# Performance work log

Hardware: AMD Instinct MI355X
Metric: run time of the kernel (lower is better)

Reference implementation:

```python
import jax, jax.numpy as jnp
import numpy as np

N_NODES = 100000
N_RELS = 8
N_EDGES = 150000
D_IN = 128
D_OUT = 128


def setup_inputs() -> dict:
    key = jax.random.key(0)
    k1, k2, k3, k4, k5 = jax.random.split(key, 5)
    scale = 1.0 / np.sqrt(D_IN)
    return {
        "x": jax.random.normal(k1, (N_NODES, D_IN), dtype=jnp.float32),
        "weight": jax.random.normal(k2, (N_RELS, D_IN, D_OUT), dtype=jnp.float32) * scale,
        "self_loop_weight": jax.random.normal(k3, (D_IN, D_OUT), dtype=jnp.float32) * scale,
        "bias": jnp.zeros((D_OUT,), dtype=jnp.float32),
        "src": jax.random.randint(k4, (N_RELS, N_EDGES), 0, N_NODES, dtype=jnp.int64),
        "dst": jax.random.randint(k5, (N_RELS, N_EDGES), 0, N_NODES, dtype=jnp.int64),
    }


def reference(x, weight, self_loop_weight, bias, src, dst):
    # Per-relation GraphConv(norm='right'): for each dst node, mean of incoming
    # src features (sum / in-degree, degree clamped to 1), then matmul W_r.
    # HeteroGraphConv sums relation outputs; then self-loop, bias, relu.
    n = x.shape[0]

    def per_rel(s, d, W):
        msgs = jax.ops.segment_sum(x[s], d, num_segments=n)          # [N, D_IN]
        deg = jax.ops.segment_sum(jnp.ones_like(s, dtype=x.dtype), d,
                                  num_segments=n)                     # [N]
        msgs = msgs / jnp.maximum(deg, 1.0)[:, None]
        return msgs @ W                                               # [N, D_OUT]

    agg = jax.vmap(per_rel)(src, dst, weight).sum(axis=0)             # [N, D_OUT]
    out = agg + x @ self_loop_weight + bias
    return jax.nn.relu(out)
```

## Files before the change

kernel.cpp:

```cpp
#include <hip/hip_runtime.h>
#include <hip/hip_bf16.h>
#include <stdint.h>

#define N_NODES 100000
#define N_RELS  8
#define N_EDGES 150000
#define KCOLS   1152
#define CAP     64

typedef short bf16x8 __attribute__((ext_vector_type(8)));
typedef float f32x4  __attribute__((ext_vector_type(4)));

__device__ __forceinline__ unsigned short f2b(float f) {
    union { float f; unsigned u; } v; v.f = f;
    unsigned r = v.u + 0x7FFF + ((v.u >> 16) & 1);
    return (unsigned short)(r >> 16);
}

__global__ void prep_w(const float* __restrict__ W, const float* __restrict__ Wself,
                       unsigned short* __restrict__ BT) {
    int flat = blockIdx.x * 256 + threadIdx.x;
    if (flat >= 128 * KCOLS) return;
    int n = flat / KCOLS, k = flat - n * KCOLS;
    float v;
    if (k < 1024) {
        int r = k >> 7, kk = k & 127;
        v = W[(r << 14) + (kk << 7) + n];
    } else {
        v = Wself[((k - 1024) << 7) + n];
    }
    BT[flat] = f2b(v);
}

__global__ void cast_x(const float* __restrict__ X, unsigned short* __restrict__ xb) {
    int t = blockIdx.x * 256 + threadIdx.x;
    if (t >= N_NODES * 16) return;
    const float4* p = (const float4*)(X + (size_t)t * 8);
    float4 a = p[0], b = p[1];
    unsigned short o[8] = { f2b(a.x), f2b(a.y), f2b(a.z), f2b(a.w),
                            f2b(b.x), f2b(b.y), f2b(b.z), f2b(b.w) };
    *(int4*)(xb + (size_t)t * 8) = *(const int4*)o;
}

__global__ void edge_build(const int* __restrict__ src, const int* __restrict__ dst,
                           int* __restrict__ cnt, int* __restrict__ ebuf) {
    int e = blockIdx.x * 256 + threadIdx.x;
    int r = blockIdx.y;
    if (e >= N_EDGES) return;
    int s = src[r * N_EDGES + e];
    int d = dst[r * N_EDGES + e];
    int slot = atomicAdd(&cnt[d], 1);
    if (slot < CAP) ebuf[d * CAP + slot] = (r << 17) | s;
}

__global__ __launch_bounds__(256) void agg_x(
    const unsigned short* __restrict__ xb, const int* __restrict__ ebuf,
    const int* __restrict__ cnt, unsigned short* __restrict__ Agg) {
    int d = (blockIdx.x << 2) + (threadIdx.x >> 6);
    if (d >= N_NODES) return;
    int lane = threadIdx.x & 63;

    int k = cnt[d]; if (k > CAP) k = CAP;
    int rec = (lane < k) ? ebuf[d * CAP + lane] : -1;
    int rl = rec >> 17;

    const unsigned int* xw = (const unsigned int*)xb;

    unsigned long long mask[8];
#pragma unroll
    for (int r = 0; r < 8; ++r) mask[r] = __ballot(rl == r);

    float ax[8], ay[8];
#pragma unroll
    for (int r = 0; r < 8; ++r) { ax[r] = 0.f; ay[r] = 0.f; }

#pragma unroll
    for (int r = 0; r < 8; ++r) {
        unsigned long long m = mask[r];
        while (m) {
            int idx = (int)__builtin_ctzll(m);
            m &= m - 1;
            int rc = __builtin_amdgcn_readlane(rec, idx);
            int s  = rc & 0x1FFFF;
            unsigned int y2 = xw[(size_t)s * 64 + lane];
            union { unsigned u; float f; } vx, vy;
            vx.u = y2 << 16;
            vy.u = y2 & 0xFFFF0000u;
            ax[r] += vx.f;
            ay[r] += vy.f;
        }
    }

#pragma unroll
    for (int r = 0; r < 8; ++r) {
        int dg = __popcll(mask[r]);
        float invr = 1.0f / (float)(dg < 1 ? 1 : dg);
        unsigned short lo = f2b(ax[r] * invr);
        unsigned short hi = f2b(ay[r] * invr);
        unsigned int pk = (unsigned int)lo | ((unsigned int)hi << 16);
        *(unsigned int*)&Agg[(size_t)d * 1024 + (r << 7) + (lane << 1)] = pk;
    }
}

__global__ __launch_bounds__(256) void gemm_out(
    const unsigned short* __restrict__ Agg, const unsigned short* __restrict__ xb,
    const unsigned short* __restrict__ BT, const float* __restrict__ bias,
    float* __restrict__ out) {
    __shared__ short As[128 * 136];
    __shared__ short Bs[128 * 136];
    int t = threadIdx.x;
    int rowBase = blockIdx.x * 128;

    int w = t >> 6, lane = t & 63;
    int wr = w >> 1, wc = w & 1;
    int ml = lane & 15, quad = lane >> 4;

    f32x4 acc[4][4];
#pragma unroll
    for (int i = 0; i < 4; ++i)
#pragma unroll
        for (int j = 0; j < 4; ++j)
            acc[i][j] = (f32x4){0.f, 0.f, 0.f, 0.f};

    for (int kc = 0; kc < 9; ++kc) {
#pragma unroll
        for (int it = 0; it < 8; ++it) {
            int idx = t + it * 256;
            int row = idx >> 4, c = idx & 15;
            int grow = rowBase + row;
            int4 v = make_int4(0, 0, 0, 0);
            if (grow < N_NODES) {
                if (kc < 8)
                    v = *(const int4*)&Agg[(size_t)grow * 1024 + (kc << 7) + c * 8];
                else
                    v = *(const int4*)&xb[(size_t)grow * 128 + c * 8];
            }
            *(int4*)&As[row * 136 + c * 8] = v;
        }
#pragma unroll
        for (int it = 0; it < 8; ++it) {
            int idx = t + it * 256;
            int n = idx >> 4, c = idx & 15;
            *(int4*)&Bs[n * 136 + c * 8] =
                *(const int4*)&BT[(size_t)n * KCOLS + (kc << 7) + c * 8];
        }
        __syncthreads();

#pragma unroll
        for (int kb = 0; kb < 4; ++kb) {
            int ko = kb * 32 + quad * 8;
            bf16x8 a[4], b[4];
#pragma unroll
            for (int i = 0; i < 4; ++i)
                a[i] = *(const bf16x8*)&As[(wr * 64 + i * 16 + ml) * 136 + ko];
#pragma unroll
            for (int j = 0; j < 4; ++j)
                b[j] = *(const bf16x8*)&Bs[(wc * 64 + j * 16 + ml) * 136 + ko];
#pragma unroll
            for (int i = 0; i < 4; ++i)
#pragma unroll
                for (int j = 0; j < 4; ++j)
                    acc[i][j] = __builtin_amdgcn_mfma_f32_16x16x32_bf16(a[i], b[j], acc[i][j], 0, 0, 0);
        }
        __syncthreads();
    }

#pragma unroll
    for (int i = 0; i < 4; ++i) {
#pragma unroll
        for (int j = 0; j < 4; ++j) {
            int col = wc * 64 + j * 16 + ml;
            float bv = bias[col];
#pragma unroll
            for (int rr = 0; rr < 4; ++rr) {
                int row = rowBase + wr * 64 + i * 16 + quad * 4 + rr;
                if (row < N_NODES) {
                    float v = acc[i][j][rr] + bv;
                    out[(size_t)row * 128 + col] = fmaxf(v, 0.f);
                }
            }
        }
    }
}

extern "C" void kernel_launch(void* const* d_in, const int* in_sizes, int n_in,
                              void* d_out, int out_size, void* d_ws, size_t ws_size,
                              hipStream_t stream) {
    const float* x     = (const float*)d_in[0];
    const float* W     = (const float*)d_in[1];
    const float* Wself = (const float*)d_in[2];
    const float* bias  = (const float*)d_in[3];
    const int*   src   = (const int*)d_in[4];
    const int*   dst   = (const int*)d_in[5];
    float* out = (float*)d_out;

    char* ws = (char*)d_ws;
    size_t off = 0;
    unsigned short* Agg = (unsigned short*)(ws + off); off += (size_t)N_NODES * 1024 * 2;
    unsigned short* xb  = (unsigned short*)(ws + off); off += (size_t)N_NODES * 128 * 2;
    unsigned short* BT  = (unsigned short*)(ws + off); off += (size_t)128 * KCOLS * 2;
    int* cnt  = (int*)(ws + off); off += (size_t)N_NODES * 4;
    int* ebuf = (int*)(ws + off); off += (size_t)N_NODES * CAP * 4;

    hipMemsetAsync(cnt, 0, (size_t)N_NODES * 4, stream);

    prep_w<<<(128 * KCOLS + 255) / 256, 256, 0, stream>>>(W, Wself, BT);
    cast_x<<<(N_NODES * 16 + 255) / 256, 256, 0, stream>>>(x, xb);

    dim3 eg((N_EDGES + 255) / 256, N_RELS);
    edge_build<<<eg, 256, 0, stream>>>(src, dst, cnt, ebuf);

    agg_x<<<(N_NODES + 3) / 4, 256, 0, stream>>>(xb, ebuf, cnt, Agg);

    gemm_out<<<(N_NODES + 127) / 128, 256, 0, stream>>>(Agg, xb, BT, bias, out);
}
```

Before: 390.6 us.

## Double-buffer GEMM tiles via direct global-to-LDS loads with XOR-swizzled layouts

The GEMM now stages its A and B tiles through global_load_lds straight into LDS, with two buffers of 64-wide K halves, so the next tile loads while MFMAs run on the current one. To keep LDS reads free of bank conflicts without padding, the layouts of BT, xb and Agg are XOR-swizzled when they are produced, and the gather in agg_x unswizzles source rows to match. This removes register staging and the serialized load-then-compute step, at the cost of coupling every producer kernel to the swizzle, twice as many K steps and barriers, and clamped out-of-range rows that load real data.

Result: faster. 361.3 us (-7.5%).

```diff
diff --git a/kernel.cpp b/kernel.cpp
--- a/kernel.cpp
+++ b/kernel.cpp
@@ -10,12 +10,21 @@
 
 typedef short bf16x8 __attribute__((ext_vector_type(8)));
 typedef float f32x4  __attribute__((ext_vector_type(4)));
+typedef unsigned int u32;
 
 __device__ __forceinline__ unsigned short f2b(float f) {
     union { float f; unsigned u; } v; v.f = f;
     unsigned r = v.u + 0x7FFF + ((v.u >> 16) & 1);
     return (unsigned short)(r >> 16);
 }
+
+__device__ __forceinline__ void gld16(const void* g, void* lds_uniform) {
+    __builtin_amdgcn_global_load_lds(
+        (const __attribute__((address_space(1))) u32*)g,
+        (__attribute__((address_space(3))) u32*)lds_uniform,
+        16, 0, 0);
+}
+
 
 __global__ void prep_w(const float* __restrict__ W, const float* __restrict__ Wself,
                        unsigned short* __restrict__ BT) {
@@ -29,17 +38,20 @@
     } else {
         v = Wself[((k - 1024) << 7) + n];
     }
-    BT[flat] = f2b(v);
+    int ks = (k & ~63) | ((k & 63) ^ ((n & 7) << 3));
+    BT[(size_t)n * KCOLS + ks] = f2b(v);
 }
 
 __global__ void cast_x(const float* __restrict__ X, unsigned short* __restrict__ xb) {
     int t = blockIdx.x * 256 + threadIdx.x;
     if (t >= N_NODES * 16) return;
-    const float4* p = (const float4*)(X + (size_t)t * 8);
+    int row = t >> 4, g = t & 15;
+    const float4* p = (const float4*)(X + (size_t)row * 128 + g * 8);
     float4 a = p[0], b = p[1];
     unsigned short o[8] = { f2b(a.x), f2b(a.y), f2b(a.z), f2b(a.w),
                             f2b(b.x), f2b(b.y), f2b(b.z), f2b(b.w) };
-    *(int4*)(xb + (size_t)t * 8) = *(const int4*)o;
+    int g2 = (g & 8) | ((g & 7) ^ (row & 7));
+    *(int4*)(xb + (size_t)row * 128 + (g2 << 3)) = *(const int4*)o;
 }
 
 __global__ void edge_build(const int* __restrict__ src, const int* __restrict__ dst,
@@ -82,7 +94,7 @@
             m &= m - 1;
             int rc = __builtin_amdgcn_readlane(rec, idx);
             int s  = rc & 0x1FFFF;
-            unsigned int y2 = xw[(size_t)s * 64 + lane];
+            unsigned int y2 = xw[(size_t)s * 64 + (lane ^ ((s & 7) << 2))];
             union { unsigned u; float f; } vx, vy;
             vx.u = y2 << 16;
             vy.u = y2 & 0xFFFF0000u;
@@ -91,6 +103,7 @@
         }
     }
 
+    int sw = (lane ^ ((d & 7) << 2)) << 1;
 #pragma unroll
     for (int r = 0; r < 8; ++r) {
         int dg = __popcll(mask[r]);
@@ -98,7 +111,7 @@
         unsigned short lo = f2b(ax[r] * invr);
         unsigned short hi = f2b(ay[r] * invr);
         unsigned int pk = (unsigned int)lo | ((unsigned int)hi << 16);
-        *(unsigned int*)&Agg[(size_t)d * 1024 + (r << 7) + (lane << 1)] = pk;
+        *(unsigned int*)&Agg[(size_t)d * 1024 + (r << 7) + sw] = pk;
     }
 }
 
@@ -106,14 +119,18 @@
     const unsigned short* __restrict__ Agg, const unsigned short* __restrict__ xb,
     const unsigned short* __restrict__ BT, const float* __restrict__ bias,
     float* __restrict__ out) {
-    __shared__ short As[128 * 136];
-    __shared__ short Bs[128 * 136];
+    __shared__ short As[2][128 * 64];
+    __shared__ short Bs[2][128 * 64];
     int t = threadIdx.x;
     int rowBase = blockIdx.x * 128;
 
     int w = t >> 6, lane = t & 63;
     int wr = w >> 1, wc = w & 1;
     int ml = lane & 15, quad = lane >> 4;
+    int sa = (lane & 7) << 4;
+
+    int ri = lane >> 3;
+    int cb = (lane & 7) << 4;
 
     f32x4 acc[4][4];
 #pragma unroll
@@ -122,47 +139,54 @@
         for (int j = 0; j < 4; ++j)
             acc[i][j] = (f32x4){0.f, 0.f, 0.f, 0.f};
 
-    for (int kc = 0; kc < 9; ++kc) {
-#pragma unroll
-        for (int it = 0; it < 8; ++it) {
-            int idx = t + it * 256;
-            int row = idx >> 4, c = idx & 15;
+    auto stage = [&](int buf, int t2) {
+        int kc = t2 >> 1, h = t2 & 1;
+#pragma unroll
+        for (int j = 0; j < 4; ++j) {
+            int i = (w << 2) + j;
+            int row = (i << 3) + ri;
             int grow = rowBase + row;
-            int4 v = make_int4(0, 0, 0, 0);
-            if (grow < N_NODES) {
-                if (kc < 8)
-                    v = *(const int4*)&Agg[(size_t)grow * 1024 + (kc << 7) + c * 8];
-                else
-                    v = *(const int4*)&xb[(size_t)grow * 128 + c * 8];
-            }
-            *(int4*)&As[row * 136 + c * 8] = v;
-        }
-#pragma unroll
-        for (int it = 0; it < 8; ++it) {
-            int idx = t + it * 256;
-            int n = idx >> 4, c = idx & 15;
-            *(int4*)&Bs[n * 136 + c * 8] =
-                *(const int4*)&BT[(size_t)n * KCOLS + (kc << 7) + c * 8];
-        }
-        __syncthreads();
-
-#pragma unroll
-        for (int kb = 0; kb < 4; ++kb) {
-            int ko = kb * 32 + quad * 8;
+            if (grow > N_NODES - 1) grow = N_NODES - 1;
+            const char* ga = (kc < 8)
+                ? (const char*)Agg + (size_t)grow * 2048 + (kc << 8) + (h << 7) + cb
+                : (const char*)xb  + (size_t)grow * 256  + (h << 7) + cb;
+            gld16(ga, (char*)&As[buf][0] + (i << 10));
+            const char* gb = (const char*)BT + (size_t)row * 2304 + (t2 << 7) + cb;
+            gld16(gb, (char*)&Bs[buf][0] + (i << 10));
+        }
+    };
+
+    auto compute = [&](int buf) {
+#pragma unroll
+        for (int kb = 0; kb < 2; ++kb) {
+            int off = ((kb << 6) + (quad << 4)) ^ sa;
             bf16x8 a[4], b[4];
 #pragma unroll
             for (int i = 0; i < 4; ++i)
-                a[i] = *(const bf16x8*)&As[(wr * 64 + i * 16 + ml) * 136 + ko];
+                a[i] = *(const bf16x8*)((const char*)&As[buf][0] +
+                        (((wr << 6) + (i << 4) + ml) << 7) + off);
 #pragma unroll
             for (int j = 0; j < 4; ++j)
-                b[j] = *(const bf16x8*)&Bs[(wc * 64 + j * 16 + ml) * 136 + ko];
+                b[j] = *(const bf16x8*)((const char*)&Bs[buf][0] +
+                        (((wc << 6) + (j << 4) + ml) << 7) + off);
 #pragma unroll
             for (int i = 0; i < 4; ++i)
 #pragma unroll
                 for (int j = 0; j < 4; ++j)
                     acc[i][j] = __builtin_amdgcn_mfma_f32_16x16x32_bf16(a[i], b[j], acc[i][j], 0, 0, 0);
         }
+    };
+
+    stage(0, 0);
+    asm volatile("s_waitcnt vmcnt(0)" ::: "memory");
+    __syncthreads();
+    int cur = 0;
+    for (int t2 = 0; t2 < 18; ++t2) {
+        if (t2 + 1 < 18) stage(cur ^ 1, t2 + 1);
+        compute(cur);
+        asm volatile("s_waitcnt vmcnt(0)" ::: "memory");
         __syncthreads();
+        cur ^= 1;
     }
 
 #pragma unroll
```

## Fuse neighbor aggregation into GEMM, dropping the intermediate Agg buffer

Applied to the files above, without the earlier changes.

Merges the aggregation kernel into the GEMM kernel. Each warp gathers and averages neighbor features for its 32 rows per relation chunk straight into an XOR-swizzled LDS tile, so the 200MB bf16 Agg buffer is never written or read back. The B operand is now read directly from global memory (BT, L2-resident) instead of staged in LDS, and launch bounds ask for 3 blocks per CU. The cost is that the edge records are reloaded for every one of the 8 relation chunks, and the serial gather loop now sits between LDS barriers with the MFMA work, so gather latency is exposed inside the GEMM blocks and there are fewer independent warps to hide it.

New measurement: 766.7 us. 96.3% more time.

```diff
diff --git a/kernel.cpp b/kernel.cpp
--- a/kernel.cpp
+++ b/kernel.cpp
@@ -53,67 +53,19 @@
     if (slot < CAP) ebuf[d * CAP + slot] = (r << 17) | s;
 }
 
-__global__ __launch_bounds__(256) void agg_x(
+__global__ __launch_bounds__(256, 3) void fused_out(
     const unsigned short* __restrict__ xb, const int* __restrict__ ebuf,
-    const int* __restrict__ cnt, unsigned short* __restrict__ Agg) {
-    int d = (blockIdx.x << 2) + (threadIdx.x >> 6);
-    if (d >= N_NODES) return;
-    int lane = threadIdx.x & 63;
-
-    int k = cnt[d]; if (k > CAP) k = CAP;
-    int rec = (lane < k) ? ebuf[d * CAP + lane] : -1;
-    int rl = rec >> 17;
-
-    const unsigned int* xw = (const unsigned int*)xb;
-
-    unsigned long long mask[8];
-#pragma unroll
-    for (int r = 0; r < 8; ++r) mask[r] = __ballot(rl == r);
-
-    float ax[8], ay[8];
-#pragma unroll
-    for (int r = 0; r < 8; ++r) { ax[r] = 0.f; ay[r] = 0.f; }
-
-#pragma unroll
-    for (int r = 0; r < 8; ++r) {
-        unsigned long long m = mask[r];
-        while (m) {
-            int idx = (int)__builtin_ctzll(m);
-            m &= m - 1;
-            int rc = __builtin_amdgcn_readlane(rec, idx);
-            int s  = rc & 0x1FFFF;
-            unsigned int y2 = xw[(size_t)s * 64 + lane];
-            union { unsigned u; float f; } vx, vy;
-            vx.u = y2 << 16;
-            vy.u = y2 & 0xFFFF0000u;
-            ax[r] += vx.f;
-            ay[r] += vy.f;
-        }
-    }
-
-#pragma unroll
-    for (int r = 0; r < 8; ++r) {
-        int dg = __popcll(mask[r]);
-        float invr = 1.0f / (float)(dg < 1 ? 1 : dg);
-        unsigned short lo = f2b(ax[r] * invr);
-        unsigned short hi = f2b(ay[r] * invr);
-        unsigned int pk = (unsigned int)lo | ((unsigned int)hi << 16);
-        *(unsigned int*)&Agg[(size_t)d * 1024 + (r << 7) + (lane << 1)] = pk;
-    }
-}
-
-__global__ __launch_bounds__(256) void gemm_out(
-    const unsigned short* __restrict__ Agg, const unsigned short* __restrict__ xb,
-    const unsigned short* __restrict__ BT, const float* __restrict__ bias,
-    float* __restrict__ out) {
-    __shared__ short As[128 * 136];
-    __shared__ short Bs[128 * 136];
+    const int* __restrict__ cnt, const unsigned short* __restrict__ BT,
+    const float* __restrict__ bias, float* __restrict__ out) {
+    __shared__ unsigned int As[128 * 64];
     int t = threadIdx.x;
     int rowBase = blockIdx.x * 128;
 
     int w = t >> 6, lane = t & 63;
     int wr = w >> 1, wc = w & 1;
     int ml = lane & 15, quad = lane >> 4;
+
+    const unsigned int* xw = (const unsigned int*)xb;
 
     f32x4 acc[4][4];
 #pragma unroll
@@ -122,40 +74,65 @@
         for (int j = 0; j < 4; ++j)
             acc[i][j] = (f32x4){0.f, 0.f, 0.f, 0.f};
 
+    auto loadRec = [&](int rr) -> int {
+        int d = rowBase + (w << 5) + rr;
+        if (d > N_NODES - 1) d = N_NODES - 1;
+        int k = cnt[d]; if (k > CAP) k = CAP;
+        return (lane < k) ? ebuf[d * CAP + lane] : -1;
+    };
+
     for (int kc = 0; kc < 9; ++kc) {
-#pragma unroll
-        for (int it = 0; it < 8; ++it) {
-            int idx = t + it * 256;
-            int row = idx >> 4, c = idx & 15;
-            int grow = rowBase + row;
-            int4 v = make_int4(0, 0, 0, 0);
-            if (grow < N_NODES) {
-                if (kc < 8)
-                    v = *(const int4*)&Agg[(size_t)grow * 1024 + (kc << 7) + c * 8];
-                else
-                    v = *(const int4*)&xb[(size_t)grow * 128 + c * 8];
+        if (kc < 8) {
+            int recN = loadRec(0);
+            for (int rr = 0; rr < 32; ++rr) {
+                int rec = recN;
+                if (rr < 31) recN = loadRec(rr + 1);
+                unsigned long long m = __ballot((rec >> 17) == kc);
+                int dg = __popcll(m);
+                float ax = 0.f, ay = 0.f;
+                while (m) {
+                    int idx = (int)__builtin_ctzll(m);
+                    m &= m - 1;
+                    int rc = __builtin_amdgcn_readlane(rec, idx);
+                    int s  = rc & 0x1FFFF;
+                    unsigned int y2 = xw[(size_t)s * 64 + lane];
+                    union { unsigned u; float f; } vx, vy;
+                    vx.u = y2 << 16;
+                    vy.u = y2 & 0xFFFF0000u;
+                    ax += vx.f;
+                    ay += vy.f;
+                }
+                float inv = 1.0f / (float)(dg < 1 ? 1 : dg);
+                unsigned int pk = (unsigned int)f2b(ax * inv)
+                                | ((unsigned int)f2b(ay * inv) << 16);
+                int row = (w << 5) + rr;
+                As[(row << 6) + (lane ^ ((row & 7) << 2))] = pk;
             }
-            *(int4*)&As[row * 136 + c * 8] = v;
-        }
-#pragma unroll
-        for (int it = 0; it < 8; ++it) {
-            int idx = t + it * 256;
-            int n = idx >> 4, c = idx & 15;
-            *(int4*)&Bs[n * 136 + c * 8] =
-                *(const int4*)&BT[(size_t)n * KCOLS + (kc << 7) + c * 8];
+        } else {
+            for (int rr = 0; rr < 32; ++rr) {
+                int row = (w << 5) + rr;
+                int d = rowBase + row;
+                if (d > N_NODES - 1) d = N_NODES - 1;
+                As[(row << 6) + (lane ^ ((row & 7) << 2))] = xw[(size_t)d * 64 + lane];
+            }
         }
         __syncthreads();
 
 #pragma unroll
         for (int kb = 0; kb < 4; ++kb) {
-            int ko = kb * 32 + quad * 8;
+            int ko = (kb << 5) + (quad << 3);
             bf16x8 a[4], b[4];
 #pragma unroll
-            for (int i = 0; i < 4; ++i)
-                a[i] = *(const bf16x8*)&As[(wr * 64 + i * 16 + ml) * 136 + ko];
+            for (int i = 0; i < 4; ++i) {
+                int row = (wr << 6) + (i << 4) + ml;
+                a[i] = *(const bf16x8*)((const char*)As + (row << 8)
+                        + ((ko << 1) ^ ((row & 7) << 4)));
+            }
 #pragma unroll
-            for (int j = 0; j < 4; ++j)
-                b[j] = *(const bf16x8*)&Bs[(wc * 64 + j * 16 + ml) * 136 + ko];
+            for (int j = 0; j < 4; ++j) {
+                int n = (wc << 6) + (j << 4) + ml;
+                b[j] = *(const bf16x8*)&BT[(size_t)n * KCOLS + (kc << 7) + ko];
+            }
 #pragma unroll
             for (int i = 0; i < 4; ++i)
 #pragma unroll
@@ -196,9 +173,8 @@
 
     char* ws = (char*)d_ws;
     size_t off = 0;
-    unsigned short* Agg = (unsigned short*)(ws + off); off += (size_t)N_NODES * 1024 * 2;
-    unsigned short* xb  = (unsigned short*)(ws + off); off += (size_t)N_NODES * 128 * 2;
-    unsigned short* BT  = (unsigned short*)(ws + off); off += (size_t)128 * KCOLS * 2;
+    unsigned short* xb = (unsigned short*)(ws + off); off += (size_t)N_NODES * 128 * 2;
+    unsigned short* BT = (unsigned short*)(ws + off); off += (size_t)128 * KCOLS * 2;
     int* cnt  = (int*)(ws + off); off += (size_t)N_NODES * 4;
     int* ebuf = (int*)(ws + off); off += (size_t)N_NODES * CAP * 4;
 
@@ -210,7 +186,5 @@
     dim3 eg((N_EDGES + 255) / 256, N_RELS);
     edge_build<<<eg, 256, 0, stream>>>(src, dst, cnt, ebuf);
 
-    agg_x<<<(N_NODES + 3) / 4, 256, 0, stream>>>(xb, ebuf, cnt, Agg);
-
-    gemm_out<<<(N_NODES + 127) / 128, 256, 0, stream>>>(Agg, xb, BT, bias, out);
+    fused_out<<<(N_NODES + 127) / 128, 256, 0, stream>>>(xb, ebuf, cnt, BT, bias, out);
 }
```
